# Performance work log

Hardware: AMD Instinct MI355X
Metric: run time of the kernel (lower is better)

The kernel has to match this reference:

```python
import jax, jax.numpy as jnp
import numpy as np

N, M, P = 8192, 8192, 16


def setup_inputs() -> dict:
    key = jax.random.key(0)
    k1, k2, k3, k4, k5 = jax.random.split(key, 5)
    x1 = jax.random.normal(k1, (N, P), dtype=jnp.float32)
    x2 = jax.random.normal(k2, (M, P), dtype=jnp.float32)
    # flax initializers.uniform() draws in [0, 0.01); use small scalars
    log_sigma_b = jax.random.uniform(k3, (), dtype=jnp.float32) * 0.01
    log_sigma_v = jax.random.uniform(k4, (), dtype=jnp.float32) * 0.01
    offset = jax.random.uniform(k5, (), dtype=jnp.float32) * 0.01
    return {"x1": x1, "x2": x2, "log_sigma_b": log_sigma_b,
            "log_sigma_v": log_sigma_v, "offset": offset}


def reference(x1, x2, log_sigma_b, log_sigma_v, offset):
    sigma_b = jnp.exp(log_sigma_b)
    sigma_v = jnp.exp(log_sigma_v)
    # sum_p (x1-offset)(x2-offset) as a dot product (n,p)@(p,m) -> (n,m)
    d = jnp.einsum("np,mp->nm", x1 - offset, x2 - offset)
    K = sigma_v ** 2 * d + sigma_b ** 2
    return K
```

## Files before the change

### kernel.cpp

```cpp
#include <hip/hip_runtime.h>
#include <cmath>


#define TILE 128
#define LDST 132

__global__ __launch_bounds__(256) void linear_kernel(
    const float* __restrict__ x1, const float* __restrict__ x2,
    const float* __restrict__ p_lsb, const float* __restrict__ p_lsv,
    const float* __restrict__ p_off, float* __restrict__ out, int ldout)
{
    __shared__ float s1[16 * LDST];
    __shared__ float s2[16 * LDST];

    const int tid = threadIdx.x;
    const int tx = tid & 15;
    const int ty = tid >> 4;
    const int n0 = blockIdx.y * TILE;
    const int m0 = blockIdx.x * TILE;

    const float off = p_off[0];
    const float sb  = expf(p_lsb[0]);
    const float sv  = expf(p_lsv[0]);
    const float sv2 = sv * sv;
    const float sb2 = sb * sb;

    const float4* g1 = (const float4*)(x1 + (size_t)n0 * 16);
    const float4* g2 = (const float4*)(x2 + (size_t)m0 * 16);
    #pragma unroll
    for (int j = tid; j < 512; j += 256) {
        const int row = j >> 2;
        const int p0  = (j & 3) * 4;
        float4 v = g1[j];
        s1[(p0 + 0) * LDST + row] = v.x - off;
        s1[(p0 + 1) * LDST + row] = v.y - off;
        s1[(p0 + 2) * LDST + row] = v.z - off;
        s1[(p0 + 3) * LDST + row] = v.w - off;
        float4 w = g2[j];
        s2[(p0 + 0) * LDST + row] = w.x - off;
        s2[(p0 + 1) * LDST + row] = w.y - off;
        s2[(p0 + 2) * LDST + row] = w.z - off;
        s2[(p0 + 3) * LDST + row] = w.w - off;
    }

    float acc[8][8];
    #pragma unroll
    for (int r = 0; r < 8; ++r)
        #pragma unroll
        for (int c = 0; c < 8; ++c) acc[r][c] = 0.0f;

    __syncthreads();

    #pragma unroll
    for (int p = 0; p < 16; ++p) {
        const float* s1p = &s1[p * LDST];
        const float* s2p = &s2[p * LDST];
        const float4 a0 = *(const float4*)&s1p[ty * 4];
        const float4 a1 = *(const float4*)&s1p[64 + ty * 4];
        const float4 b0 = *(const float4*)&s2p[tx * 4];
        const float4 b1 = *(const float4*)&s2p[64 + tx * 4];
        const float av[8] = {a0.x, a0.y, a0.z, a0.w, a1.x, a1.y, a1.z, a1.w};
        const float bv[8] = {b0.x, b0.y, b0.z, b0.w, b1.x, b1.y, b1.z, b1.w};
        #pragma unroll
        for (int r = 0; r < 8; ++r)
            #pragma unroll
            for (int c = 0; c < 8; ++c)
                acc[r][c] += av[r] * bv[c];
    }

    #pragma unroll
    for (int r = 0; r < 8; ++r) {
        const int lr  = (r < 4) ? (ty * 4 + r) : (64 + ty * 4 + (r - 4));
        float* orow = out + (size_t)(n0 + lr) * (size_t)ldout + m0;
        float4 o0, o1;
        o0.x = sv2 * acc[r][0] + sb2;
        o0.y = sv2 * acc[r][1] + sb2;
        o0.z = sv2 * acc[r][2] + sb2;
        o0.w = sv2 * acc[r][3] + sb2;
        o1.x = sv2 * acc[r][4] + sb2;
        o1.y = sv2 * acc[r][5] + sb2;
        o1.z = sv2 * acc[r][6] + sb2;
        o1.w = sv2 * acc[r][7] + sb2;
        *(float4*)&orow[tx * 4]      = o0;
        *(float4*)&orow[64 + tx * 4] = o1;
    }
}

extern "C" void kernel_launch(void* const* d_in, const int* in_sizes, int n_in,
                              void* d_out, int out_size, void* d_ws, size_t ws_size,
                              hipStream_t stream) {
    const float* x1  = (const float*)d_in[0];
    const float* x2  = (const float*)d_in[1];
    const float* lsb = (const float*)d_in[2];
    const float* lsv = (const float*)d_in[3];
    const float* off = (const float*)d_in[4];
    float* out = (float*)d_out;

    const int n = in_sizes[0] / 16;
    const int m = in_sizes[1] / 16;

    dim3 grid(m / TILE, n / TILE);
    linear_kernel<<<grid, 256, 0, stream>>>(x1, x2, lsb, lsv, off, out, m);
}
```

Before: 274.3 us.

## Restructure into row-strip blocks streaming x2 chunks with nontemporal stores

Each block now owns 16 output rows, keeps its x1 rows in registers, and loops over the M dimension in 512-column chunks staged through shared memory. Output is written with nontemporal vector stores, so full contiguous row segments are emitted and cache pollution from the large output is avoided. In exchange, every block re-reads all of x2, there are syncs per chunk, and the grid is smaller, with less register tiling per thread.

```diff
diff --git a/kernel.cpp b/kernel.cpp
--- a/kernel.cpp
+++ b/kernel.cpp
@@ -2,22 +2,23 @@
 #include <cmath>
 
 
-#define TILE 128
-#define LDST 132
+#define ROWS  16
+#define CHUNK 512
+#define LDST  516
 
-__global__ __launch_bounds__(256) void linear_kernel(
+typedef float floatx4 __attribute__((ext_vector_type(4)));
+
+__global__ __launch_bounds__(512, 4) void linear_kernel(
     const float* __restrict__ x1, const float* __restrict__ x2,
     const float* __restrict__ p_lsb, const float* __restrict__ p_lsv,
-    const float* __restrict__ p_off, float* __restrict__ out, int ldout)
+    const float* __restrict__ p_off, float* __restrict__ out, int M)
 {
-    __shared__ float s1[16 * LDST];
     __shared__ float s2[16 * LDST];
 
     const int tid = threadIdx.x;
-    const int tx = tid & 15;
-    const int ty = tid >> 4;
-    const int n0 = blockIdx.y * TILE;
-    const int m0 = blockIdx.x * TILE;
+    const int tx = tid & 127;
+    const int ty = tid >> 7;
+    const int n0 = blockIdx.x * ROWS;
 
     const float off = p_off[0];
     const float sb  = expf(p_lsb[0]);
@@ -25,64 +26,68 @@
     const float sv2 = sv * sv;
     const float sb2 = sb * sb;
 
-    const float4* g1 = (const float4*)(x1 + (size_t)n0 * 16);
-    const float4* g2 = (const float4*)(x2 + (size_t)m0 * 16);
+    float a[4][16];
     #pragma unroll
-    for (int j = tid; j < 512; j += 256) {
-        const int row = j >> 2;
-        const int p0  = (j & 3) * 4;
-        float4 v = g1[j];
-        s1[(p0 + 0) * LDST + row] = v.x - off;
-        s1[(p0 + 1) * LDST + row] = v.y - off;
-        s1[(p0 + 2) * LDST + row] = v.z - off;
-        s1[(p0 + 3) * LDST + row] = v.w - off;
-        float4 w = g2[j];
-        s2[(p0 + 0) * LDST + row] = w.x - off;
-        s2[(p0 + 1) * LDST + row] = w.y - off;
-        s2[(p0 + 2) * LDST + row] = w.z - off;
-        s2[(p0 + 3) * LDST + row] = w.w - off;
+    for (int r = 0; r < 4; ++r) {
+        const float4* g = (const float4*)(x1 + (size_t)(n0 + ty * 4 + r) * 16);
+        #pragma unroll
+        for (int q = 0; q < 4; ++q) {
+            float4 v = g[q];
+            a[r][q * 4 + 0] = v.x - off;
+            a[r][q * 4 + 1] = v.y - off;
+            a[r][q * 4 + 2] = v.z - off;
+            a[r][q * 4 + 3] = v.w - off;
+        }
     }
 
-    float acc[8][8];
-    #pragma unroll
-    for (int r = 0; r < 8; ++r)
+    const int nchunks = M / CHUNK;
+    for (int ch = 0; ch < nchunks; ++ch) {
+        const int m0 = ch * CHUNK;
+
+        const float4* g2 = (const float4*)(x2 + (size_t)m0 * 16);
         #pragma unroll
-        for (int c = 0; c < 8; ++c) acc[r][c] = 0.0f;
+        for (int i = 0; i < 4; ++i) {
+            const int j   = i * 512 + tid;
+            const int row = j >> 2;
+            const int p0  = (j & 3) * 4;
+            float4 v = g2[j];
+            s2[(p0 + 0) * LDST + row] = v.x - off;
+            s2[(p0 + 1) * LDST + row] = v.y - off;
+            s2[(p0 + 2) * LDST + row] = v.z - off;
+            s2[(p0 + 3) * LDST + row] = v.w - off;
+        }
+        __syncthreads();
 
-    __syncthreads();
+        float acc[4][4];
+        #pragma unroll
+        for (int r = 0; r < 4; ++r)
+            #pragma unroll
+            for (int c = 0; c < 4; ++c) acc[r][c] = 0.0f;
 
-    #pragma unroll
-    for (int p = 0; p < 16; ++p) {
-        const float* s1p = &s1[p * LDST];
-        const float* s2p = &s2[p * LDST];
-        const float4 a0 = *(const float4*)&s1p[ty * 4];
-        const float4 a1 = *(const float4*)&s1p[64 + ty * 4];
-        const float4 b0 = *(const float4*)&s2p[tx * 4];
-        const float4 b1 = *(const float4*)&s2p[64 + tx * 4];
-        const float av[8] = {a0.x, a0.y, a0.z, a0.w, a1.x, a1.y, a1.z, a1.w};
-        const float bv[8] = {b0.x, b0.y, b0.z, b0.w, b1.x, b1.y, b1.z, b1.w};
         #pragma unroll
-        for (int r = 0; r < 8; ++r)
+        for (int p = 0; p < 16; ++p) {
+            const float4 b = *(const float4*)&s2[p * LDST + tx * 4];
+            const float bv[4] = {b.x, b.y, b.z, b.w};
             #pragma unroll
-            for (int c = 0; c < 8; ++c)
-                acc[r][c] += av[r] * bv[c];
-    }
+            for (int r = 0; r < 4; ++r)
+                #pragma unroll
+                for (int c = 0; c < 4; ++c)
+                    acc[r][c] += a[r][p] * bv[c];
+        }
 
-    #pragma unroll
-    for (int r = 0; r < 8; ++r) {
-        const int lr  = (r < 4) ? (ty * 4 + r) : (64 + ty * 4 + (r - 4));
-        float* orow = out + (size_t)(n0 + lr) * (size_t)ldout + m0;
-        float4 o0, o1;
-        o0.x = sv2 * acc[r][0] + sb2;
-        o0.y = sv2 * acc[r][1] + sb2;
-        o0.z = sv2 * acc[r][2] + sb2;
-        o0.w = sv2 * acc[r][3] + sb2;
-        o1.x = sv2 * acc[r][4] + sb2;
-        o1.y = sv2 * acc[r][5] + sb2;
-        o1.z = sv2 * acc[r][6] + sb2;
-        o1.w = sv2 * acc[r][7] + sb2;
-        *(float4*)&orow[tx * 4]      = o0;
-        *(float4*)&orow[64 + tx * 4] = o1;
+        __syncthreads();
+
+        #pragma unroll
+        for (int r = 0; r < 4; ++r) {
+            floatx4 o;
+            o.x = sv2 * acc[r][0] + sb2;
+            o.y = sv2 * acc[r][1] + sb2;
+            o.z = sv2 * acc[r][2] + sb2;
+            o.w = sv2 * acc[r][3] + sb2;
+            floatx4* dst = (floatx4*)(out + (size_t)(n0 + ty * 4 + r) * (size_t)M
+                                          + m0 + tx * 4);
+            __builtin_nontemporal_store(o, dst);
+        }
     }
 }
 
@@ -99,6 +104,5 @@
     const int n = in_sizes[0] / 16;
     const int m = in_sizes[1] / 16;
 
-    dim3 grid(m / TILE, n / TILE);
-    linear_kernel<<<grid, 256, 0, stream>>>(x1, x2, lsb, lsv, off, out, m);
+    linear_kernel<<<n / ROWS, 512, 0, stream>>>(x1, x2, lsb, lsv, off, out, m);
 }
```

Result: slower. 422.1 us (+53.9%).
